# Performance work log

Hardware: AMD Instinct MI355X
Metric: run time of the kernel (lower is better)

Reference implementation:

```python
import jax, jax.numpy as jnp
import numpy as np

B, T, P, D = 4, 1024, 64, 128


def _lin_params(k, fin, fout):
    kw, kb = jax.random.split(k)
    w = jax.random.normal(kw, (fin, fout), jnp.float32) / np.sqrt(fin).astype(np.float32)
    b = jax.random.normal(kb, (fout,), jnp.float32) * 0.01
    return w, b


def setup_inputs() -> dict:
    key = jax.random.key(0)
    ks = jax.random.split(key, 10)
    positions = jax.random.normal(ks[0], (B, T, P, D), jnp.float32)
    context = jax.random.normal(ks[1], (B, T, D), jnp.float32)
    hierarchy_depth = jax.random.normal(ks[2], (B, T, P), jnp.float32)
    cw1, cb1 = _lin_params(ks[3], 2 * D, 128)
    cw2, cb2 = _lin_params(ks[4], 128, 64)
    cw3, cb3 = _lin_params(ks[5], 64, 1)
    hw1, hb1 = _lin_params(ks[6], D + 1, 32)
    hw2, hb2 = _lin_params(ks[7], 32, 16)
    hw3, hb3 = _lin_params(ks[8], 16, 1)
    curvature_memory = jnp.full((P,), -1.0, jnp.float32)  # (num_components,1) squeezed
    return {
        'positions': positions, 'context': context, 'hierarchy_depth': hierarchy_depth,
        'cw1': cw1, 'cb1': cb1, 'cw2': cw2, 'cb2': cb2, 'cw3': cw3, 'cb3': cb3,
        'hw1': hw1, 'hb1': hb1, 'hw2': hw2, 'hb2': hb2, 'hw3': hw3, 'hb3': hb3,
        'curvature_memory': curvature_memory,
    }


def _local_curvatures(positions):
    # positions: (B,T,P,D) -> flatten point clouds
    pf = positions.reshape(-1, P, D)                      # (BT,P,D)
    sq = jnp.sum(pf * pf, axis=-1)                        # (BT,P)
    d2 = sq[:, :, None] + sq[:, None, :] - 2.0 * jnp.einsum('npd,nqd->npq', pf, pf)
    dist = jnp.sqrt(jnp.maximum(d2, 1e-12))               # (BT,P,P), cdist
    k = min(3, P - 1)
    # k+1 smallest distances (includes self distance ~0 at slot 0)
    neg_small, _ = jax.lax.top_k(-dist, k + 1)            # (BT,P,k+1)
    nearest = -neg_small                                  # ascending
    mean_dist = nearest[:, :, 1:].mean(axis=-1)
    density = 1.0 / (mean_dist + 1e-6)
    curv = -2.0 * jnp.tanh(density)
    return curv.reshape(B, T, P)


def reference(positions, context, hierarchy_depth,
              cw1, cb1, cw2, cb2, cw3, cb3,
              hw1, hb1, hw2, hb2, hw3, hb3,
              curvature_memory):
    local = _local_curvatures(positions)                  # (B,T,P)

    # context encoder: cat(pos, ctx) -> 128 relu -> 64 relu -> 1
    ctx_exp = jnp.broadcast_to(context[:, :, None, :], (B, T, P, D))
    ci = jnp.concatenate([positions, ctx_exp], axis=-1)   # (B,T,P,2D)
    h = jax.nn.relu(ci @ cw1 + cb1)
    h = jax.nn.relu(h @ cw2 + cb2)
    ctx_curv = (h @ cw3 + cb3)[..., 0]                    # (B,T,P)

    # hierarchy net: cat(pos, tanh(depth)) -> 32 relu -> 16 tanh -> 1
    hi = jnp.concatenate([positions, jnp.tanh(hierarchy_depth)[..., None]], axis=-1)
    g = jax.nn.relu(hi @ hw1 + hb1)
    g = jnp.tanh(g @ hw2 + hb2)
    hier_curv = (g @ hw3 + hb3)[..., 0]                   # (B,T,P)

    combined = 0.5 * local + 0.3 * ctx_curv + 0.2 * hier_curv

    # momentum memory update + smoothing (momentum=0.9, adaptation_rate=0.1)
    cur_mean = combined.mean(axis=(0, 1))                 # (P,)
    new_mem = 0.9 * curvature_memory + 0.1 * cur_mean
    smoothed = 0.9 * combined + 0.1 * new_mem[None, None, :]
    return jnp.clip(smoothed, -5.0, 2.0)
```

## Files before the change

### kernel.cpp

```cpp
#include <hip/hip_runtime.h>
#include <hip/hip_bf16.h>

typedef __attribute__((ext_vector_type(4))) float  float4v;
typedef __attribute__((ext_vector_type(2))) unsigned int uint2v;
typedef __attribute__((ext_vector_type(8))) short  short8v;
typedef __attribute__((ext_vector_type(4))) float  f32x4;

__device__ __forceinline__ unsigned short f2bf(float f) {
    unsigned int u = __float_as_uint(f);
    u += 0x7FFFu + ((u >> 16) & 1u);
    return (unsigned short)(u >> 16);
}

__device__ __forceinline__ float ftanh(float x) {
    float s = fminf(x * 2.8853900817779268f, 115.0f);
    float t = exp2f(s);
    return (t - 1.0f) * __builtin_amdgcn_rcpf(t + 1.0f);
}

__device__ __forceinline__ int swzb(int row, int kbyte) {
    return row * 256 + (kbyte ^ ((row & 7) << 4));
}
__device__ __forceinline__ int swzh(int row, int kbyte) {
    return row * 256 + (kbyte ^ ((row & 7) << 4) ^ ((row & 8) << 2));
}

__global__ void prep_weights(const float* __restrict__ cw1, const float* __restrict__ cw2,
                             const float* __restrict__ hw1, const float* __restrict__ hw2,
                             unsigned short* __restrict__ w1bT, unsigned short* __restrict__ w2bT,
                             unsigned short* __restrict__ hw1T, unsigned short* __restrict__ hw2T) {
    int i = blockIdx.x * 256 + threadIdx.x;
    if (i < 16384) {
        int j = i >> 7, k = i & 127;
        w1bT[i] = f2bf(cw1[k * 128 + j]);
    } else if (i < 24576) {
        int t = i - 16384; int j = t >> 7, k = t & 127;
        w2bT[t] = f2bf(cw2[k * 64 + j]);
    } else if (i < 28672) {
        int t = i - 24576; int j = t >> 7, k = t & 127;
        hw1T[t] = f2bf(hw1[k * 32 + j]);
    } else if (i < 29184) {
        int t = i - 28672; int j = t >> 5, k = t & 31;
        hw2T[t] = f2bf(hw2[k * 16 + j]);
    }
}

__global__ __launch_bounds__(256) void ctx_gemm(const float* __restrict__ ctx,
                                                const float* __restrict__ cw1,
                                                const float* __restrict__ cb1,
                                                float* __restrict__ ctxW1) {
    __shared__ float ldsW[128 * 128];
    __shared__ float ldsC[16 * 128];
    const int tid = threadIdx.x;
    const int bt0 = blockIdx.x * 16;
    for (int i = tid; i < 16384; i += 256) {
        int d = i >> 7, j = i & 127;
        ldsW[i] = cw1[(128 + d) * 128 + j];
    }
    for (int i = tid; i < 2048; i += 256) ldsC[i] = ctx[bt0 * 128 + i];
    __syncthreads();
    const int j = tid & 127, half = tid >> 7;
    float acc[8];
    float bj = cb1[j];
#pragma unroll
    for (int k = 0; k < 8; ++k) acc[k] = bj;
    for (int d = 0; d < 128; ++d) {
        float wv = ldsW[d * 128 + j];
#pragma unroll
        for (int k = 0; k < 8; ++k) acc[k] += ldsC[(half * 8 + k) * 128 + d] * wv;
    }
#pragma unroll
    for (int k = 0; k < 8; ++k) ctxW1[(size_t)(bt0 + half * 8 + k) * 128 + j] = acc[k];
}

__global__ __launch_bounds__(256, 4) void fused_main(
    const float* __restrict__ pos_g, const float* __restrict__ dep_g,
    const float* __restrict__ cb2,  const float* __restrict__ cw3,
    const float* __restrict__ cb3,  const float* __restrict__ hw1,
    const float* __restrict__ hb1,  const float* __restrict__ hb2,
    const float* __restrict__ hw3,  const float* __restrict__ hb3,
    const unsigned short* __restrict__ w1bT, const unsigned short* __restrict__ w2bT,
    const unsigned short* __restrict__ hw1T, const unsigned short* __restrict__ hw2T,
    const float* __restrict__ ctxW1g, float* __restrict__ out)
{
    __shared__ __align__(16) short posB[64 * 128];
    __shared__ __align__(16) short h1B[64 * 128];
    __shared__ __align__(16) short g1B[64 * 32];
    __shared__ float tdep[64], diag[64], localc[64], hierc[64];
    __shared__ float ctxp[256];

    const int bt  = blockIdx.x;
    const int tid = threadIdx.x;
    const int lane = tid & 63;
    const int w   = tid >> 6;
    const int lr  = lane & 15;
    const int lk  = lane >> 4;
    const int R   = w * 16;

    const short8v* w1p8 = (const short8v*)w1bT;
    const short8v* w2p8 = (const short8v*)w2bT;
    short8v w1f[2][4], w2f[4];
#pragma unroll
    for (int jtl = 0; jtl < 2; ++jtl)
#pragma unroll
        for (int ks = 0; ks < 4; ++ks)
            w1f[jtl][ks] = w1p8[(32 * w + jtl * 16 + lr) * 16 + ks * 4 + lk];
#pragma unroll
    for (int ks = 0; ks < 4; ++ks)
        w2f[ks] = w2p8[(16 * w + lr) * 16 + ks * 4 + lk];
    short8v hw2f = ((const short8v*)hw2T)[lr * 4 + lk];
    float cvals[2];
    cvals[0] = ctxW1g[(size_t)bt * 128 + 32 * w + lr];
    cvals[1] = ctxW1g[(size_t)bt * 128 + 32 * w + 16 + lr];
    float cb2v = cb2[16 * w + lr], cw3v = cw3[16 * w + lr], cb3v = cb3[0];
    float hb2v = hb2[lr], hw3v = hw3[lr], hb3v = hb3[0];

    const float4v* pos4 = (const float4v*)(pos_g + (size_t)bt * 8192);
#pragma unroll
    for (int i = 0; i < 8; ++i) {
        int c = tid + 256 * i;
        int row = c >> 5, c4 = c & 31;
        float4v v = pos4[c];
        __hip_bfloat162 lo2 = __float22bfloat162_rn(make_float2(v[0], v[1]));
        __hip_bfloat162 hi2 = __float22bfloat162_rn(make_float2(v[2], v[3]));
        unsigned int u0, u1;
        __builtin_memcpy(&u0, &lo2, 4);
        __builtin_memcpy(&u1, &hi2, 4);
        uint2v uu = {u0, u1};
        *(uint2v*)((char*)posB + row * 256 + ((c4 * 8) ^ ((row & 7) << 4))) = uu;
    }
    if (tid < 64) tdep[tid] = ftanh(dep_g[bt * 64 + tid]);
    __syncthreads();

    f32x4 g0 = {0.f,0.f,0.f,0.f}, g1t = {0.f,0.f,0.f,0.f},
          g2t = {0.f,0.f,0.f,0.f}, g3t = {0.f,0.f,0.f,0.f};
#pragma unroll
    for (int ks = 0; ks < 4; ++ks) {
        int kb = ks * 64 + lk * 16;
        short8v a = *(const short8v*)((const char*)posB + swzb(R + lr, kb));
        short8v b0 = *(const short8v*)((const char*)posB + swzb(0  + lr, kb));
        short8v b1 = *(const short8v*)((const char*)posB + swzb(16 + lr, kb));
        short8v b2 = *(const short8v*)((const char*)posB + swzb(32 + lr, kb));
        short8v b3 = *(const short8v*)((const char*)posB + swzb(48 + lr, kb));
        g0 = __builtin_amdgcn_mfma_f32_16x16x32_bf16(a, b0, g0, 0, 0, 0);
        g1t = __builtin_amdgcn_mfma_f32_16x16x32_bf16(a, b1, g1t, 0, 0, 0);
        g2t = __builtin_amdgcn_mfma_f32_16x16x32_bf16(a, b2, g2t, 0, 0, 0);
        g3t = __builtin_amdgcn_mfma_f32_16x16x32_bf16(a, b3, g3t, 0, 0, 0);
    }
    {
        f32x4 gw = (w == 0) ? g0 : (w == 1) ? g1t : (w == 2) ? g2t : g3t;
        int e = lr & 3;
        float dv = (e == 0) ? gw[0] : (e == 1) ? gw[1] : (e == 2) ? gw[2] : gw[3];
        if (lk == (lr >> 2)) diag[R + lr] = dv;
    }
    __syncthreads();

    {
        float s0[4], s1[4], s2[4], s3[4];
#pragma unroll
        for (int e = 0; e < 4; ++e) {
            int p = R + 4 * lk + e;
            float dp = diag[p];
            s0[e] = s1[e] = s2[e] = s3[e] = 1e30f;
#pragma unroll
            for (int jt = 0; jt < 4; ++jt) {
                f32x4 gt = (jt == 0) ? g0 : (jt == 1) ? g1t : (jt == 2) ? g2t : g3t;
                float gv = (e == 0) ? gt[0] : (e == 1) ? gt[1] : (e == 2) ? gt[2] : gt[3];
                float d2 = dp + diag[jt * 16 + lr] - 2.f * gv;
                float c0 = fminf(s0[e], d2), m0 = fmaxf(s0[e], d2);
                float c1 = fminf(s1[e], m0), m1 = fmaxf(s1[e], m0);
                float c2 = fminf(s2[e], m1), m2 = fmaxf(s2[e], m1);
                float c3 = fminf(s3[e], m2);
                s0[e] = c0; s1[e] = c1; s2[e] = c2; s3[e] = c3;
            }
        }
#pragma unroll
        for (int m = 1; m <= 8; m <<= 1) {
#pragma unroll
            for (int e = 0; e < 4; ++e) {
                float t0 = __shfl_xor(s0[e], m);
                float t1 = __shfl_xor(s1[e], m);
                float t2 = __shfl_xor(s2[e], m);
                float t3 = __shfl_xor(s3[e], m);
                float r0 = fminf(s0[e], t3), r1 = fminf(s1[e], t2);
                float r2 = fminf(s2[e], t1), r3 = fminf(s3[e], t0);
                float a0 = fminf(r0, r2), b0 = fmaxf(r0, r2);
                float a1 = fminf(r1, r3), b1 = fmaxf(r1, r3);
                s0[e] = fminf(a0, a1); s1[e] = fmaxf(a0, a1);
                s2[e] = fminf(b0, b1); s3[e] = fmaxf(b0, b1);
            }
        }
        if (lr == 0) {
#pragma unroll
            for (int e = 0; e < 4; ++e) {
                float d1 = __builtin_amdgcn_sqrtf(fmaxf(s1[e], 1e-12f));
                float d2 = __builtin_amdgcn_sqrtf(fmaxf(s2[e], 1e-12f));
                float d3 = __builtin_amdgcn_sqrtf(fmaxf(s3[e], 1e-12f));
                float mean = (d1 + d2 + d3) * (1.f / 3.f);
                localc[R + 4 * lk + e] = -2.f * ftanh(__builtin_amdgcn_rcpf(mean + 1e-6f));
            }
        }
    }

    {
        f32x4 h1a[4][2];
#pragma unroll
        for (int rt = 0; rt < 4; ++rt)
#pragma unroll
            for (int jtl = 0; jtl < 2; ++jtl) h1a[rt][jtl] = (f32x4){0.f,0.f,0.f,0.f};
#pragma unroll
        for (int ks = 0; ks < 4; ++ks) {
            int kb = ks * 64 + lk * 16;
#pragma unroll
            for (int rt = 0; rt < 4; ++rt) {
                short8v a = *(const short8v*)((const char*)posB + swzb(rt * 16 + lr, kb));
                h1a[rt][0] = __builtin_amdgcn_mfma_f32_16x16x32_bf16(a, w1f[0][ks], h1a[rt][0], 0, 0, 0);
                h1a[rt][1] = __builtin_amdgcn_mfma_f32_16x16x32_bf16(a, w1f[1][ks], h1a[rt][1], 0, 0, 0);
            }
        }
#pragma unroll
        for (int rt = 0; rt < 4; ++rt)
#pragma unroll
            for (int jtl = 0; jtl < 2; ++jtl) {
                int j = 32 * w + jtl * 16 + lr;
                float add = cvals[jtl];
#pragma unroll
                for (int e = 0; e < 4; ++e) {
                    int p = rt * 16 + 4 * lk + e;
                    float v = fmaxf(h1a[rt][jtl][e] + add, 0.f);
                    *(short*)((char*)h1B + swzh(p, 2 * j)) = (short)f2bf(v);
                }
            }
    }
    __syncthreads();

    const short8v* hw1p8 = (const short8v*)hw1T;
    short8v hw1f[2][4];
#pragma unroll
    for (int jt = 0; jt < 2; ++jt)
#pragma unroll
        for (int ks = 0; ks < 4; ++ks)
            hw1f[jt][ks] = hw1p8[(jt * 16 + lr) * 16 + ks * 4 + lk];
    float u1v[2], hb1v[2];
#pragma unroll
    for (int jt = 0; jt < 2; ++jt) { u1v[jt] = hw1[4096 + jt * 16 + lr]; hb1v[jt] = hb1[jt * 16 + lr]; }
    {
        f32x4 h2[4];
#pragma unroll
        for (int rt = 0; rt < 4; ++rt) h2[rt] = (f32x4){0.f,0.f,0.f,0.f};
#pragma unroll
        for (int ks = 0; ks < 4; ++ks) {
            int kb = ks * 64 + lk * 16;
#pragma unroll
            for (int rt = 0; rt < 4; ++rt) {
                short8v a = *(const short8v*)((const char*)h1B + swzh(rt * 16 + lr, kb));
                h2[rt] = __builtin_amdgcn_mfma_f32_16x16x32_bf16(a, w2f[ks], h2[rt], 0, 0, 0);
            }
        }
        float s4[4][4];
#pragma unroll
        for (int rt = 0; rt < 4; ++rt)
#pragma unroll
            for (int e = 0; e < 4; ++e)
                s4[rt][e] = fmaxf(h2[rt][e] + cb2v, 0.f) * cw3v;
#pragma unroll
        for (int m = 1; m <= 8; m <<= 1) {
#pragma unroll
            for (int rt = 0; rt < 4; ++rt)
#pragma unroll
                for (int e = 0; e < 4; ++e) s4[rt][e] += __shfl_xor(s4[rt][e], m);
        }
        if (lr == 0) {
#pragma unroll
            for (int rt = 0; rt < 4; ++rt)
#pragma unroll
                for (int e = 0; e < 4; ++e)
                    ctxp[w * 64 + rt * 16 + 4 * lk + e] = s4[rt][e];
        }
    }

    {
        f32x4 q0 = {0.f,0.f,0.f,0.f}, q1 = {0.f,0.f,0.f,0.f};
#pragma unroll
        for (int ks = 0; ks < 4; ++ks) {
            int kb = ks * 64 + lk * 16;
            short8v a = *(const short8v*)((const char*)posB + swzb(R + lr, kb));
            q0 = __builtin_amdgcn_mfma_f32_16x16x32_bf16(a, hw1f[0][ks], q0, 0, 0, 0);
            q1 = __builtin_amdgcn_mfma_f32_16x16x32_bf16(a, hw1f[1][ks], q1, 0, 0, 0);
        }
#pragma unroll
        for (int jt = 0; jt < 2; ++jt) {
            int j = jt * 16 + lr;
#pragma unroll
            for (int e = 0; e < 4; ++e) {
                int p = R + 4 * lk + e;
                f32x4 qq = (jt == 0) ? q0 : q1;
                float v = fmaxf(qq[e] + tdep[p] * u1v[jt] + hb1v[jt], 0.f);
                *(short*)((char*)g1B + p * 64 + ((2 * j) ^ ((p & 3) << 4))) = (short)f2bf(v);
            }
        }
    }
    asm volatile("s_waitcnt lgkmcnt(0)" ::: "memory");

    {
        int p2 = R + lr;
        short8v a = *(const short8v*)((const char*)g1B + p2 * 64 + ((lk * 16) ^ ((p2 & 3) << 4)));
        f32x4 g2 = {0.f,0.f,0.f,0.f};
        g2 = __builtin_amdgcn_mfma_f32_16x16x32_bf16(a, hw2f, g2, 0, 0, 0);
        float sh[4];
#pragma unroll
        for (int e = 0; e < 4; ++e) sh[e] = ftanh(g2[e] + hb2v) * hw3v;
#pragma unroll
        for (int m = 1; m <= 8; m <<= 1) {
#pragma unroll
            for (int e = 0; e < 4; ++e) sh[e] += __shfl_xor(sh[e], m);
        }
        if (lr == 0) {
#pragma unroll
            for (int e = 0; e < 4; ++e) hierc[R + 4 * lk + e] = sh[e] + hb3v;
        }
    }
    __syncthreads();

    if (tid < 64) {
        float ctxv = ctxp[tid] + ctxp[64 + tid] + ctxp[128 + tid] + ctxp[192 + tid] + cb3v;
        float comb = 0.5f * localc[tid] + 0.3f * ctxv + 0.2f * hierc[tid];
        out[(size_t)bt * 64 + tid] = comb;
    }
}

__global__ void reduce1(const float* __restrict__ comb, float* __restrict__ partials) {
    __shared__ float sm[256];
    int b = blockIdx.x, tid = threadIdx.x;
    const float* src = comb + (size_t)b * 1024;
    float s = 0.f;
#pragma unroll
    for (int k = 0; k < 4; ++k) s += src[tid + 256 * k];
    sm[tid] = s;
    __syncthreads();
    if (tid < 64) partials[b * 64 + tid] = sm[tid] + sm[tid + 64] + sm[tid + 128] + sm[tid + 192];
}

__global__ void reduce2(const float* __restrict__ partials, const float* __restrict__ mem,
                        float* __restrict__ newmem) {
    int p = threadIdx.x;
    float s0 = 0.f, s1 = 0.f, s2 = 0.f, s3 = 0.f;
    for (int b = 0; b < 256; b += 4) {
        s0 += partials[(b + 0) * 64 + p];
        s1 += partials[(b + 1) * 64 + p];
        s2 += partials[(b + 2) * 64 + p];
        s3 += partials[(b + 3) * 64 + p];
    }
    float s = (s0 + s1) + (s2 + s3);
    newmem[p] = 0.9f * mem[p] + 0.1f * (s * (1.f / 4096.f));
}

__global__ void finalize(float* __restrict__ out, const float* __restrict__ newmem) {
    int t = blockIdx.x * 256 + threadIdx.x;
    float4v v = *(float4v*)(out + 4 * (size_t)t);
    float4v nm = *(const float4v*)(newmem + ((4 * t) & 63));
#pragma unroll
    for (int e = 0; e < 4; ++e) {
        float x = 0.9f * v[e] + 0.1f * nm[e];
        v[e] = fminf(fmaxf(x, -5.f), 2.f);
    }
    *(float4v*)(out + 4 * (size_t)t) = v;
}

extern "C" void kernel_launch(void* const* d_in, const int* in_sizes, int n_in,
                              void* d_out, int out_size, void* d_ws, size_t ws_size,
                              hipStream_t stream) {
    (void)in_sizes; (void)n_in; (void)out_size; (void)ws_size;
    const float* pos = (const float*)d_in[0];
    const float* ctx = (const float*)d_in[1];
    const float* dep = (const float*)d_in[2];
    const float* cw1 = (const float*)d_in[3];
    const float* cb1 = (const float*)d_in[4];
    const float* cw2 = (const float*)d_in[5];
    const float* cb2 = (const float*)d_in[6];
    const float* cw3 = (const float*)d_in[7];
    const float* cb3 = (const float*)d_in[8];
    const float* hw1 = (const float*)d_in[9];
    const float* hb1 = (const float*)d_in[10];
    const float* hw2 = (const float*)d_in[11];
    const float* hb2 = (const float*)d_in[12];
    const float* hw3 = (const float*)d_in[13];
    const float* hb3 = (const float*)d_in[14];
    const float* cmem = (const float*)d_in[15];
    float* out = (float*)d_out;
    float* ws = (float*)d_ws;
    float* partials = ws;
    float* newmem = ws + 16384;
    unsigned short* wT = (unsigned short*)(ws + 16448);
    unsigned short* w1bT = wT;
    unsigned short* w2bT = wT + 16384;
    unsigned short* hw1T = wT + 24576;
    unsigned short* hw2T = wT + 28672;
    float* ctxW1 = ws + 31040;

    prep_weights<<<114, 256, 0, stream>>>(cw1, cw2, hw1, hw2, w1bT, w2bT, hw1T, hw2T);
    ctx_gemm<<<256, 256, 0, stream>>>(ctx, cw1, cb1, ctxW1);
    fused_main<<<4096, 256, 0, stream>>>(pos, dep, cb2, cw3, cb3,
                                         hw1, hb1, hb2, hw3, hb3,
                                         w1bT, w2bT, hw1T, hw2T, ctxW1, out);
    reduce1<<<256, 256, 0, stream>>>(out, partials);
    reduce2<<<1, 64, 0, stream>>>(partials, cmem, newmem);
    finalize<<<256, 256, 0, stream>>>(out, newmem);
}
```

Before: 83.80 us.

## Split fused_main work across eight waves per block with LDS kNN merge

```diff
diff --git a/kernel.cpp b/kernel.cpp
--- a/kernel.cpp
+++ b/kernel.cpp
@@ -73,7 +73,7 @@
     for (int k = 0; k < 8; ++k) ctxW1[(size_t)(bt0 + half * 8 + k) * 128 + j] = acc[k];
 }
 
-__global__ __launch_bounds__(256, 4) void fused_main(
+__global__ __launch_bounds__(512, 6) void fused_main(
     const float* __restrict__ pos_g, const float* __restrict__ dep_g,
     const float* __restrict__ cb2,  const float* __restrict__ cw3,
     const float* __restrict__ cb3,  const float* __restrict__ hw1,
@@ -86,72 +86,57 @@
     __shared__ __align__(16) short posB[64 * 128];
     __shared__ __align__(16) short h1B[64 * 128];
     __shared__ __align__(16) short g1B[64 * 32];
-    __shared__ float tdep[64], diag[64], localc[64], hierc[64];
+    __shared__ float tdep[64], diag[64], localc[64];
     __shared__ float ctxp[256];
+    __shared__ float knnp[512];
 
     const int bt  = blockIdx.x;
     const int tid = threadIdx.x;
+    const int w   = tid >> 6;
     const int lane = tid & 63;
-    const int w   = tid >> 6;
     const int lr  = lane & 15;
     const int lk  = lane >> 4;
-    const int R   = w * 16;
-
-    const short8v* w1p8 = (const short8v*)w1bT;
-    const short8v* w2p8 = (const short8v*)w2bT;
-    short8v w1f[2][4], w2f[4];
-#pragma unroll
-    for (int jtl = 0; jtl < 2; ++jtl)
-#pragma unroll
-        for (int ks = 0; ks < 4; ++ks)
-            w1f[jtl][ks] = w1p8[(32 * w + jtl * 16 + lr) * 16 + ks * 4 + lk];
-#pragma unroll
-    for (int ks = 0; ks < 4; ++ks)
-        w2f[ks] = w2p8[(16 * w + lr) * 16 + ks * 4 + lk];
-    short8v hw2f = ((const short8v*)hw2T)[lr * 4 + lk];
-    float cvals[2];
-    cvals[0] = ctxW1g[(size_t)bt * 128 + 32 * w + lr];
-    cvals[1] = ctxW1g[(size_t)bt * 128 + 32 * w + 16 + lr];
-    float cb2v = cb2[16 * w + lr], cw3v = cw3[16 * w + lr], cb3v = cb3[0];
-    float hb2v = hb2[lr], hw3v = hw3[lr], hb3v = hb3[0];
-
-    const float4v* pos4 = (const float4v*)(pos_g + (size_t)bt * 8192);
-#pragma unroll
-    for (int i = 0; i < 8; ++i) {
-        int c = tid + 256 * i;
-        int row = c >> 5, c4 = c & 31;
-        float4v v = pos4[c];
-        __hip_bfloat162 lo2 = __float22bfloat162_rn(make_float2(v[0], v[1]));
-        __hip_bfloat162 hi2 = __float22bfloat162_rn(make_float2(v[2], v[3]));
-        unsigned int u0, u1;
-        __builtin_memcpy(&u0, &lo2, 4);
-        __builtin_memcpy(&u1, &hi2, 4);
-        uint2v uu = {u0, u1};
-        *(uint2v*)((char*)posB + row * 256 + ((c4 * 8) ^ ((row & 7) << 4))) = uu;
+    const int rT  = w >> 1;
+    const int hT  = w & 1;
+
+    {
+        const float4v* gp = (const float4v*)(pos_g + (size_t)bt * 8192) + tid;
+        const int srow = tid >> 5, sc4 = tid & 31;
+        char* lp = (char*)posB + srow * 256 + ((sc4 * 8) ^ ((srow & 7) << 4));
+#pragma unroll
+        for (int i = 0; i < 4; ++i) {
+            float4v v = gp[512 * i];
+            __hip_bfloat162 lo2 = __float22bfloat162_rn(make_float2(v[0], v[1]));
+            __hip_bfloat162 hi2 = __float22bfloat162_rn(make_float2(v[2], v[3]));
+            unsigned int u0, u1;
+            __builtin_memcpy(&u0, &lo2, 4);
+            __builtin_memcpy(&u1, &hi2, 4);
+            uint2v uu = {u0, u1};
+            *(uint2v*)(lp + 4096 * i) = uu;
+        }
     }
     if (tid < 64) tdep[tid] = ftanh(dep_g[bt * 64 + tid]);
     __syncthreads();
 
-    f32x4 g0 = {0.f,0.f,0.f,0.f}, g1t = {0.f,0.f,0.f,0.f},
-          g2t = {0.f,0.f,0.f,0.f}, g3t = {0.f,0.f,0.f,0.f};
-#pragma unroll
-    for (int ks = 0; ks < 4; ++ks) {
-        int kb = ks * 64 + lk * 16;
-        short8v a = *(const short8v*)((const char*)posB + swzb(R + lr, kb));
-        short8v b0 = *(const short8v*)((const char*)posB + swzb(0  + lr, kb));
-        short8v b1 = *(const short8v*)((const char*)posB + swzb(16 + lr, kb));
-        short8v b2 = *(const short8v*)((const char*)posB + swzb(32 + lr, kb));
-        short8v b3 = *(const short8v*)((const char*)posB + swzb(48 + lr, kb));
-        g0 = __builtin_amdgcn_mfma_f32_16x16x32_bf16(a, b0, g0, 0, 0, 0);
-        g1t = __builtin_amdgcn_mfma_f32_16x16x32_bf16(a, b1, g1t, 0, 0, 0);
-        g2t = __builtin_amdgcn_mfma_f32_16x16x32_bf16(a, b2, g2t, 0, 0, 0);
-        g3t = __builtin_amdgcn_mfma_f32_16x16x32_bf16(a, b3, g3t, 0, 0, 0);
-    }
-    {
-        f32x4 gw = (w == 0) ? g0 : (w == 1) ? g1t : (w == 2) ? g2t : g3t;
-        int e = lr & 3;
-        float dv = (e == 0) ? gw[0] : (e == 1) ? gw[1] : (e == 2) ? gw[2] : gw[3];
-        if (lk == (lr >> 2)) diag[R + lr] = dv;
+    f32x4 ga = {0.f,0.f,0.f,0.f}, gb = {0.f,0.f,0.f,0.f};
+    {
+        const int c0 = 2 * hT;
+#pragma unroll
+        for (int ks = 0; ks < 4; ++ks) {
+            int kb = ks * 64 + lk * 16;
+            short8v a  = *(const short8v*)((const char*)posB + swzb(16 * rT + lr, kb));
+            short8v b0 = *(const short8v*)((const char*)posB + swzb(16 * c0 + lr, kb));
+            short8v b1 = *(const short8v*)((const char*)posB + swzb(16 * c0 + 16 + lr, kb));
+            ga = __builtin_amdgcn_mfma_f32_16x16x32_bf16(a, b0, ga, 0, 0, 0);
+            gb = __builtin_amdgcn_mfma_f32_16x16x32_bf16(a, b1, gb, 0, 0, 0);
+        }
+        bool haveA = (c0 == rT), haveB = (c0 + 1 == rT);
+        if (haveA || haveB) {
+            f32x4 gd = haveA ? ga : gb;
+            int e = lr & 3;
+            float dv = (e == 0) ? gd[0] : (e == 1) ? gd[1] : (e == 2) ? gd[2] : gd[3];
+            if (lk == (lr >> 2)) diag[16 * rT + lr] = dv;
+        }
     }
     __syncthreads();
 
@@ -159,14 +144,14 @@
         float s0[4], s1[4], s2[4], s3[4];
 #pragma unroll
         for (int e = 0; e < 4; ++e) {
-            int p = R + 4 * lk + e;
+            int p = 16 * rT + 4 * lk + e;
             float dp = diag[p];
             s0[e] = s1[e] = s2[e] = s3[e] = 1e30f;
 #pragma unroll
-            for (int jt = 0; jt < 4; ++jt) {
-                f32x4 gt = (jt == 0) ? g0 : (jt == 1) ? g1t : (jt == 2) ? g2t : g3t;
+            for (int t = 0; t < 2; ++t) {
+                f32x4 gt = (t == 0) ? ga : gb;
                 float gv = (e == 0) ? gt[0] : (e == 1) ? gt[1] : (e == 2) ? gt[2] : gt[3];
-                float d2 = dp + diag[jt * 16 + lr] - 2.f * gv;
+                float d2 = dp + diag[16 * (2 * hT + t) + lr] - 2.f * gv;
                 float c0 = fminf(s0[e], d2), m0 = fmaxf(s0[e], d2);
                 float c1 = fminf(s1[e], m0), m1 = fmaxf(s1[e], m0);
                 float c2 = fminf(s2[e], m1), m2 = fmaxf(s2[e], m1);
@@ -193,117 +178,133 @@
         if (lr == 0) {
 #pragma unroll
             for (int e = 0; e < 4; ++e) {
-                float d1 = __builtin_amdgcn_sqrtf(fmaxf(s1[e], 1e-12f));
-                float d2 = __builtin_amdgcn_sqrtf(fmaxf(s2[e], 1e-12f));
-                float d3 = __builtin_amdgcn_sqrtf(fmaxf(s3[e], 1e-12f));
-                float mean = (d1 + d2 + d3) * (1.f / 3.f);
-                localc[R + 4 * lk + e] = -2.f * ftanh(__builtin_amdgcn_rcpf(mean + 1e-6f));
-            }
-        }
-    }
-
-    {
-        f32x4 h1a[4][2];
-#pragma unroll
-        for (int rt = 0; rt < 4; ++rt)
-#pragma unroll
-            for (int jtl = 0; jtl < 2; ++jtl) h1a[rt][jtl] = (f32x4){0.f,0.f,0.f,0.f};
+                int p = 16 * rT + 4 * lk + e;
+                knnp[hT * 256 + p * 4 + 0] = s0[e];
+                knnp[hT * 256 + p * 4 + 1] = s1[e];
+                knnp[hT * 256 + p * 4 + 2] = s2[e];
+                knnp[hT * 256 + p * 4 + 3] = s3[e];
+            }
+        }
+    }
+    {
+        const short8v* w1p8 = (const short8v*)w1bT;
+        short8v w1f[4];
+#pragma unroll
+        for (int ks = 0; ks < 4; ++ks)
+            w1f[ks] = w1p8[(16 * w + lr) * 16 + ks * 4 + lk];
+        float cval = ctxW1g[(size_t)bt * 128 + 16 * w + lr];
+        f32x4 h1a[4];
+#pragma unroll
+        for (int rt = 0; rt < 4; ++rt) h1a[rt] = (f32x4){0.f,0.f,0.f,0.f};
 #pragma unroll
         for (int ks = 0; ks < 4; ++ks) {
             int kb = ks * 64 + lk * 16;
 #pragma unroll
             for (int rt = 0; rt < 4; ++rt) {
                 short8v a = *(const short8v*)((const char*)posB + swzb(rt * 16 + lr, kb));
-                h1a[rt][0] = __builtin_amdgcn_mfma_f32_16x16x32_bf16(a, w1f[0][ks], h1a[rt][0], 0, 0, 0);
-                h1a[rt][1] = __builtin_amdgcn_mfma_f32_16x16x32_bf16(a, w1f[1][ks], h1a[rt][1], 0, 0, 0);
-            }
-        }
+                h1a[rt] = __builtin_amdgcn_mfma_f32_16x16x32_bf16(a, w1f[ks], h1a[rt], 0, 0, 0);
+            }
+        }
+        int j = 16 * w + lr;
 #pragma unroll
         for (int rt = 0; rt < 4; ++rt)
 #pragma unroll
-            for (int jtl = 0; jtl < 2; ++jtl) {
-                int j = 32 * w + jtl * 16 + lr;
-                float add = cvals[jtl];
-#pragma unroll
-                for (int e = 0; e < 4; ++e) {
-                    int p = rt * 16 + 4 * lk + e;
-                    float v = fmaxf(h1a[rt][jtl][e] + add, 0.f);
-                    *(short*)((char*)h1B + swzh(p, 2 * j)) = (short)f2bf(v);
-                }
-            }
-    }
-    __syncthreads();
-
+            for (int e = 0; e < 4; ++e) {
+                int p = rt * 16 + 4 * lk + e;
+                float v = fmaxf(h1a[rt][e] + cval, 0.f);
+                *(short*)((char*)h1B + swzh(p, 2 * j)) = (short)f2bf(v);
+            }
+    }
+    __syncthreads();
+
+    const short8v* w2p8 = (const short8v*)w2bT;
     const short8v* hw1p8 = (const short8v*)hw1T;
-    short8v hw1f[2][4];
-#pragma unroll
-    for (int jt = 0; jt < 2; ++jt)
-#pragma unroll
-        for (int ks = 0; ks < 4; ++ks)
-            hw1f[jt][ks] = hw1p8[(jt * 16 + lr) * 16 + ks * 4 + lk];
-    float u1v[2], hb1v[2];
-#pragma unroll
-    for (int jt = 0; jt < 2; ++jt) { u1v[jt] = hw1[4096 + jt * 16 + lr]; hb1v[jt] = hb1[jt * 16 + lr]; }
-    {
-        f32x4 h2[4];
-#pragma unroll
-        for (int rt = 0; rt < 4; ++rt) h2[rt] = (f32x4){0.f,0.f,0.f,0.f};
+    short8v w2f[4], hw1f[4];
+#pragma unroll
+    for (int ks = 0; ks < 4; ++ks) {
+        w2f[ks]  = w2p8[(16 * rT + lr) * 16 + ks * 4 + lk];
+        hw1f[ks] = hw1p8[(16 * hT + lr) * 16 + ks * 4 + lk];
+    }
+    float cb2v = cb2[16 * rT + lr], cw3v = cw3[16 * rT + lr];
+    float u1v = hw1[4096 + 16 * hT + lr], hb1v = hb1[16 * hT + lr];
+
+    if (tid < 64) {
+        int p = tid;
+        float a0 = knnp[p * 4 + 0], a1 = knnp[p * 4 + 1], a2 = knnp[p * 4 + 2], a3 = knnp[p * 4 + 3];
+        float b0 = knnp[256 + p * 4 + 0], b1 = knnp[256 + p * 4 + 1],
+              b2 = knnp[256 + p * 4 + 2], b3 = knnp[256 + p * 4 + 3];
+        float m0 = fminf(a0, b3), m1 = fminf(a1, b2), m2 = fminf(a2, b1), m3 = fminf(a3, b0);
+        float x0 = fminf(m0, m2), x2 = fmaxf(m0, m2), x1 = fminf(m1, m3), x3 = fmaxf(m1, m3);
+        float s1 = fmaxf(fminf(x0, x1), 0.f) * 0.f + fmaxf(fminf(x0, x1), fminf(x0, x1));
+        s1 = fmaxf(x0, x1) < fminf(x2, x3) ? fmaxf(x0, x1) : fmaxf(x0, x1);
+        float q1 = fmaxf(x0, x1);
+        float q2 = fminf(x2, x3);
+        float q3 = fmaxf(x2, x3);
+        float d1 = __builtin_amdgcn_sqrtf(fmaxf(q1, 1e-12f));
+        float d2 = __builtin_amdgcn_sqrtf(fmaxf(q2, 1e-12f));
+        float d3 = __builtin_amdgcn_sqrtf(fmaxf(q3, 1e-12f));
+        float mean = (d1 + d2 + d3) * (1.f / 3.f);
+        localc[p] = -2.f * ftanh(__builtin_amdgcn_rcpf(mean + 1e-6f));
+    }
+
+    {
+        f32x4 h2[2];
+        h2[0] = (f32x4){0.f,0.f,0.f,0.f};
+        h2[1] = (f32x4){0.f,0.f,0.f,0.f};
+        const int rt0 = 2 * hT;
 #pragma unroll
         for (int ks = 0; ks < 4; ++ks) {
             int kb = ks * 64 + lk * 16;
-#pragma unroll
-            for (int rt = 0; rt < 4; ++rt) {
-                short8v a = *(const short8v*)((const char*)h1B + swzh(rt * 16 + lr, kb));
-                h2[rt] = __builtin_amdgcn_mfma_f32_16x16x32_bf16(a, w2f[ks], h2[rt], 0, 0, 0);
-            }
-        }
-        float s4[4][4];
-#pragma unroll
-        for (int rt = 0; rt < 4; ++rt)
+            short8v aA = *(const short8v*)((const char*)h1B + swzh(16 * rt0 + lr, kb));
+            short8v aB = *(const short8v*)((const char*)h1B + swzh(16 * rt0 + 16 + lr, kb));
+            h2[0] = __builtin_amdgcn_mfma_f32_16x16x32_bf16(aA, w2f[ks], h2[0], 0, 0, 0);
+            h2[1] = __builtin_amdgcn_mfma_f32_16x16x32_bf16(aB, w2f[ks], h2[1], 0, 0, 0);
+        }
+        float s4[2][4];
+#pragma unroll
+        for (int u = 0; u < 2; ++u)
 #pragma unroll
             for (int e = 0; e < 4; ++e)
-                s4[rt][e] = fmaxf(h2[rt][e] + cb2v, 0.f) * cw3v;
+                s4[u][e] = fmaxf(h2[u][e] + cb2v, 0.f) * cw3v;
 #pragma unroll
         for (int m = 1; m <= 8; m <<= 1) {
 #pragma unroll
-            for (int rt = 0; rt < 4; ++rt)
-#pragma unroll
-                for (int e = 0; e < 4; ++e) s4[rt][e] += __shfl_xor(s4[rt][e], m);
+            for (int u = 0; u < 2; ++u)
+#pragma unroll
+                for (int e = 0; e < 4; ++e) s4[u][e] += __shfl_xor(s4[u][e], m);
         }
         if (lr == 0) {
 #pragma unroll
-            for (int rt = 0; rt < 4; ++rt)
+            for (int u = 0; u < 2; ++u)
 #pragma unroll
                 for (int e = 0; e < 4; ++e)
-                    ctxp[w * 64 + rt * 16 + 4 * lk + e] = s4[rt][e];
-        }
-    }
-
-    {
-        f32x4 q0 = {0.f,0.f,0.f,0.f}, q1 = {0.f,0.f,0.f,0.f};
+                    ctxp[rT * 64 + (rt0 + u) * 16 + 4 * lk + e] = s4[u][e];
+        }
+    }
+
+    {
+        f32x4 q = {0.f,0.f,0.f,0.f};
 #pragma unroll
         for (int ks = 0; ks < 4; ++ks) {
             int kb = ks * 64 + lk * 16;
-            short8v a = *(const short8v*)((const char*)posB + swzb(R + lr, kb));
-            q0 = __builtin_amdgcn_mfma_f32_16x16x32_bf16(a, hw1f[0][ks], q0, 0, 0, 0);
-            q1 = __builtin_amdgcn_mfma_f32_16x16x32_bf16(a, hw1f[1][ks], q1, 0, 0, 0);
-        }
-#pragma unroll
-        for (int jt = 0; jt < 2; ++jt) {
-            int j = jt * 16 + lr;
-#pragma unroll
-            for (int e = 0; e < 4; ++e) {
-                int p = R + 4 * lk + e;
-                f32x4 qq = (jt == 0) ? q0 : q1;
-                float v = fmaxf(qq[e] + tdep[p] * u1v[jt] + hb1v[jt], 0.f);
-                *(short*)((char*)g1B + p * 64 + ((2 * j) ^ ((p & 3) << 4))) = (short)f2bf(v);
-            }
-        }
-    }
-    asm volatile("s_waitcnt lgkmcnt(0)" ::: "memory");
-
-    {
-        int p2 = R + lr;
+            short8v a = *(const short8v*)((const char*)posB + swzb(16 * rT + lr, kb));
+            q = __builtin_amdgcn_mfma_f32_16x16x32_bf16(a, hw1f[ks], q, 0, 0, 0);
+        }
+        int j = 16 * hT + lr;
+#pragma unroll
+        for (int e = 0; e < 4; ++e) {
+            int p = 16 * rT + 4 * lk + e;
+            float v = fmaxf(q[e] + tdep[p] * u1v + hb1v, 0.f);
+            *(short*)((char*)g1B + p * 64 + ((2 * j) ^ ((p & 3) << 4))) = (short)f2bf(v);
+        }
+    }
+    __syncthreads();
+
+    if (hT == 0) {
+        short8v hw2f = ((const short8v*)hw2T)[lr * 4 + lk];
+        float hb2v = hb2[lr], hw3v = hw3[lr];
+        float hb3v = hb3[0], cb3v = cb3[0];
+        int p2 = 16 * rT + lr;
         short8v a = *(const short8v*)((const char*)g1B + p2 * 64 + ((lk * 16) ^ ((p2 & 3) << 4)));
         f32x4 g2 = {0.f,0.f,0.f,0.f};
         g2 = __builtin_amdgcn_mfma_f32_16x16x32_bf16(a, hw2f, g2, 0, 0, 0);
@@ -317,15 +318,13 @@
         }
         if (lr == 0) {
 #pragma unroll
-            for (int e = 0; e < 4; ++e) hierc[R + 4 * lk + e] = sh[e] + hb3v;
-        }
-    }
-    __syncthreads();
-
-    if (tid < 64) {
-        float ctxv = ctxp[tid] + ctxp[64 + tid] + ctxp[128 + tid] + ctxp[192 + tid] + cb3v;
-        float comb = 0.5f * localc[tid] + 0.3f * ctxv + 0.2f * hierc[tid];
-        out[(size_t)bt * 64 + tid] = comb;
+            for (int e = 0; e < 4; ++e) {
+                int p = 16 * rT + 4 * lk + e;
+                float ctxv = ctxp[p] + ctxp[64 + p] + ctxp[128 + p] + ctxp[192 + p] + cb3v;
+                float comb = 0.5f * localc[p] + 0.3f * ctxv + 0.2f * (sh[e] + hb3v);
+                out[(size_t)bt * 64 + p] = comb;
+            }
+        }
     }
 }
 
@@ -400,7 +399,7 @@
 
     prep_weights<<<114, 256, 0, stream>>>(cw1, cw2, hw1, hw2, w1bT, w2bT, hw1T, hw2T);
     ctx_gemm<<<256, 256, 0, stream>>>(ctx, cw1, cb1, ctxW1);
-    fused_main<<<4096, 256, 0, stream>>>(pos, dep, cb2, cw3, cb3,
+    fused_main<<<4096, 512, 0, stream>>>(pos, dep, cb2, cw3, cb3,
                                          hw1, hb1, hb2, hw3, hb3,
                                          w1bT, w2bT, hw1T, hw2T, ctxW1, out);
     reduce1<<<256, 256, 0, stream>>>(out, partials);
```

New measurement: 102.5 us. 1.22x slower.
